# Performance work log

Measured on AMD Instinct MI355X. Metric: run time of the kernel, lower is better.

The kernel has to match this reference:

```python
import jax, jax.numpy as jnp
import numpy as np

TRIANGLE_TABLE = jnp.array([
    [-1, -1, -1, -1, -1, -1], [1, 0, 2, -1, -1, -1], [4, 0, 3, -1, -1, -1],
    [1, 4, 2, 1, 3, 4], [3, 1, 5, -1, -1, -1], [2, 3, 0, 2, 5, 3],
    [1, 4, 0, 1, 5, 4], [4, 2, 5, -1, -1, -1], [4, 5, 2, -1, -1, -1],
    [4, 1, 0, 4, 5, 1], [3, 2, 0, 3, 5, 2], [1, 3, 5, -1, -1, -1],
    [4, 1, 2, 4, 3, 1], [3, 0, 4, -1, -1, -1], [2, 0, 1, -1, -1, -1],
    [-1, -1, -1, -1, -1, -1]], dtype=jnp.int32)
NUM_TRI_TABLE = jnp.array([0, 1, 1, 2, 1, 2, 2, 1, 1, 2, 2, 1, 2, 1, 1, 0], dtype=jnp.int32)
BASE_TET_EDGES = jnp.array([0, 1, 0, 2, 0, 3, 1, 2, 1, 3, 2, 3], dtype=jnp.int32)

NUM_VERTS = 500_000
NUM_TETS = 2_000_000


def setup_inputs() -> dict:
    key = jax.random.key(0)
    k1, k2, k3 = jax.random.split(key, 3)
    pos_nx3 = jax.random.normal(k1, (NUM_VERTS, 3), dtype=jnp.float32)
    sdf_n = jax.random.normal(k2, (NUM_VERTS,), dtype=jnp.float32)
    tet_fx4 = jax.random.randint(k3, (NUM_TETS, 4), 0, NUM_VERTS)
    return {"pos_nx3": pos_nx3, "sdf_n": sdf_n, "tet_fx4": tet_fx4}


def _map_uv(face_gidx, max_idx):
    N = int(np.ceil(np.sqrt((max_idx + 1) // 2)))
    lin = jnp.linspace(0.0, 1.0 - 1.0 / N, N, dtype=jnp.float32)
    tex_y, tex_x = jnp.meshgrid(lin, lin, indexing='ij')
    pad = 0.9 / N
    # (N, N, 8) -> (N*N*4, 2): 4 uv corners per texel
    uvs = jnp.stack([tex_x, tex_y, tex_x + pad, tex_y,
                     tex_x + pad, tex_y + pad, tex_x, tex_y + pad], axis=-1).reshape(-1, 2)
    tet_idx = face_gidx // 2
    x = tet_idx % N
    y = tet_idx // N
    tet_idx = y * N + x
    tri_idx = face_gidx % 2
    uv_idx = jnp.stack([tet_idx * 4, tet_idx * 4 + tri_idx + 1,
                        tet_idx * 4 + tri_idx + 2], axis=-1).reshape(-1, 3)
    return uvs, uv_idx


def reference(pos_nx3, sdf_n, tet_fx4):
    # --- topology extraction (non-differentiable, data-dependent shapes; eager) ---
    occ_n = sdf_n > 0                                  # (N,)
    occ_fx4 = occ_n[tet_fx4]                           # (F, 4)
    occ_sum = occ_fx4.sum(-1)
    valid = (occ_sum > 0) & (occ_sum < 4)              # surface-crossing tets
    tets_v = tet_fx4[valid]                            # (Fv, 4)

    e = tets_v[:, BASE_TET_EDGES].reshape(-1, 2)       # (Fv*6, 2)
    e = jnp.stack([jnp.minimum(e[:, 0], e[:, 1]),
                   jnp.maximum(e[:, 0], e[:, 1])], axis=-1)  # sorted edges
    unique_edges, idx_map = jnp.unique(e, axis=0, return_inverse=True)
    idx_map = idx_map.reshape(-1)

    mask_edges = occ_n[unique_edges].sum(-1) == 1      # edges crossing surface
    mapping = jnp.where(mask_edges, jnp.cumsum(mask_edges) - 1, -1)
    idx_map = mapping[idx_map].reshape(-1, 6)          # (Fv, 6) per-tet edge->vert id
    interp_v = unique_edges[mask_edges]                # (E, 2)

    # --- differentiable vertex interpolation ---
    p = pos_nx3[interp_v]                              # (E, 2, 3)
    signs = jnp.array([[1.0], [-1.0]], dtype=pos_nx3.dtype)
    s = sdf_n[interp_v][..., None] * signs             # (E, 2, 1), second negated
    w = jnp.flip(s, axis=1) / s.sum(1, keepdims=True)
    verts = (p * w).sum(1)                             # (E, 3)

    # --- triangulation via lookup table ---
    v_id = jnp.array([1, 2, 4, 8], dtype=jnp.int32)
    tetindex = (occ_fx4[valid].astype(jnp.int32) * v_id).sum(-1)  # (Fv,)
    ntri = NUM_TRI_TABLE[tetindex]
    m1 = ntri == 1
    m2 = ntri == 2
    f1 = jnp.take_along_axis(idx_map[m1], TRIANGLE_TABLE[tetindex[m1]][:, :3], axis=1).reshape(-1, 3)
    f2 = jnp.take_along_axis(idx_map[m2], TRIANGLE_TABLE[tetindex[m2]][:, :6], axis=1).reshape(-1, 3)
    faces = jnp.concatenate([f1, f2], axis=0)

    num_tets = tet_fx4.shape[0]
    tet_gidx = jnp.arange(num_tets)[valid]
    g2 = tet_gidx[m2] * 2
    face_gidx = jnp.concatenate([tet_gidx[m1] * 2,
                                 jnp.stack([g2, g2 + 1], axis=-1).reshape(-1)], axis=0)
    uvs, uv_idx = _map_uv(face_gidx, num_tets * 2)
    return verts, faces, uvs, uv_idx
```

## Files before the change

### kernel.cpp

```cpp
#include <hip/hip_runtime.h>
#include <stdint.h>
#include <math.h>

#define SB 256
#define SI 8
#define SCHUNK (SB*SI)
#define C2 2048
#define LDSN (C2 + 256)
#define HEADBIT 0x40000000u
#define VMASK   0x3FFFFFFFu

__constant__ int c_tri[16][6] = {
  {-1,-1,-1,-1,-1,-1},{1,0,2,-1,-1,-1},{4,0,3,-1,-1,-1},{1,4,2,1,3,4},
  {3,1,5,-1,-1,-1},{2,3,0,2,5,3},{1,4,0,1,5,4},{4,2,5,-1,-1,-1},
  {4,5,2,-1,-1,-1},{4,1,0,4,5,1},{3,2,0,3,5,2},{1,3,5,-1,-1,-1},
  {4,1,2,4,3,1},{3,0,4,-1,-1,-1},{2,0,1,-1,-1,-1},{-1,-1,-1,-1,-1,-1}};
__constant__ int c_ntri[16] = {0,1,1,2,1,2,2,1,1,2,2,1,2,1,1,0};
__constant__ int c_ea[6] = {0,0,0,1,1,2};
__constant__ int c_eb[6] = {1,2,3,2,3,3};

__global__ void k_classify(const int4* __restrict__ tet, const float* __restrict__ sdf,
                           uint8_t* __restrict__ tetidx, int* __restrict__ bucketCnt,
                           ushort4* __restrict__ stash, int nt) {
  int t = blockIdx.x * blockDim.x + threadIdx.x;
  if (t >= nt) return;
  int4 v = tet[t];
  int ids[4] = {v.x, v.y, v.z, v.w};
  int bits = 0;
#pragma unroll
  for (int i = 0; i < 4; i++) bits |= (sdf[ids[i]] > 0.0f) ? (1 << i) : 0;
  tetidx[t] = (uint8_t)bits;
  if (c_ntri[bits] == 0) return;
  int los[4];
  int c = 0;
#pragma unroll
  for (int e = 0; e < 6; e++) {
    int a = c_ea[e], b = c_eb[e];
    if ((((bits >> a) ^ (bits >> b)) & 1) == 0) continue;
    int va = ids[a], vb = ids[b];
    los[c++] = va < vb ? va : vb;
  }
  unsigned short st[4] = {0, 0, 0, 0};
  unsigned done = 0;
#pragma unroll
  for (int i = 0; i < 4; i++) {
    if (i >= c || (done & (1u << i))) continue;
    int cnt = 1;
#pragma unroll
    for (int j = 1; j < 4; j++)
      if (i + j < c && los[i + j] == los[i]) cnt++;
    int base = atomicAdd(&bucketCnt[los[i]], cnt);
    int k = 0;
#pragma unroll
    for (int j = 0; j < 4; j++) {
      if (i + j < c && los[i + j] == los[i]) {
        st[i + j] = (unsigned short)(base + k);
        k++;
        done |= 1u << (i + j);
      }
    }
  }
  stash[t] = make_ushort4(st[0], st[1], st[2], st[3]);
}

__device__ inline unsigned long long blkExclU64(unsigned long long val, unsigned long long* sh) {
  int tid = threadIdx.x;
  sh[tid] = val; __syncthreads();
  for (int st = 1; st < SB; st <<= 1) {
    unsigned long long add = (tid >= st) ? sh[tid - st] : 0ull;
    __syncthreads();
    sh[tid] += add;
    __syncthreads();
  }
  return sh[tid] - val;
}
__device__ inline int blkExclI32(int val, int* sh) {
  int tid = threadIdx.x;
  sh[tid] = val; __syncthreads();
  for (int st = 1; st < SB; st <<= 1) {
    int add = (tid >= st) ? sh[tid - st] : 0;
    __syncthreads();
    sh[tid] += add;
    __syncthreads();
  }
  return sh[tid] - val;
}

__global__ void k_pass1(const uint8_t* __restrict__ tetidx, int nt,
                        const int* __restrict__ bucketCnt, int nv,
                        unsigned long long* __restrict__ btU, int* __restrict__ btI, int nb_t) {
  __shared__ unsigned long long shU[SB];
  int* shI = (int*)shU;
  if ((int)blockIdx.x < nb_t) {
    int base = blockIdx.x * SCHUNK + threadIdx.x * SI;
    unsigned long long s = 0;
    for (int k = 0; k < SI; k++) {
      int i = base + k;
      if (i < nt) {
        int n3 = c_ntri[tetidx[i]];
        s += (n3 == 1 ? 1ull : 0ull) + (n3 == 2 ? (1ull << 32) : 0ull);
      }
    }
    shU[threadIdx.x] = s; __syncthreads();
    for (int st = SB / 2; st > 0; st >>= 1) {
      if (threadIdx.x < st) shU[threadIdx.x] += shU[threadIdx.x + st];
      __syncthreads();
    }
    if (threadIdx.x == 0) btU[blockIdx.x] = shU[0];
  } else {
    int bid = blockIdx.x - nb_t;
    int base = bid * SCHUNK + threadIdx.x * SI;
    int s = 0;
    for (int k = 0; k < SI; k++) { int i = base + k; if (i < nv) s += bucketCnt[i]; }
    shI[threadIdx.x] = s; __syncthreads();
    for (int st = SB / 2; st > 0; st >>= 1) {
      if (threadIdx.x < st) shI[threadIdx.x] += shI[threadIdx.x + st];
      __syncthreads();
    }
    if (threadIdx.x == 0) btI[bid] = shI[0];
  }
}

__global__ void k_scanmid(unsigned long long* __restrict__ btU, int nbU,
                          int* __restrict__ btI, int nbI, int* __restrict__ scal) {
  __shared__ unsigned long long shU[SB];
  __shared__ unsigned long long carryU;
  int* shI = (int*)shU;
  __shared__ int carryI;
  if (blockIdx.x == 0) {
    if (threadIdx.x == 0) carryU = 0;
    __syncthreads();
    for (int base = 0; base < nbU; base += SB) {
      int i = base + threadIdx.x;
      unsigned long long v = (i < nbU) ? btU[i] : 0ull;
      unsigned long long ex = blkExclU64(v, shU);
      unsigned long long carry = carryU;
      if (i < nbU) btU[i] = carry + ex;
      __syncthreads();
      if (threadIdx.x == SB - 1) carryU = carry + ex + v;
      __syncthreads();
    }
    if (threadIdx.x == 0) {
      scal[0] = (int)(carryU & 0xffffffffull);
      scal[1] = (int)(carryU >> 32);
    }
  } else {
    if (threadIdx.x == 0) carryI = 0;
    __syncthreads();
    for (int base = 0; base < nbI; base += SB) {
      int i = base + threadIdx.x;
      int v = (i < nbI) ? btI[i] : 0;
      int ex = blkExclI32(v, shI);
      int carry = carryI;
      if (i < nbI) btI[i] = carry + ex;
      __syncthreads();
      if (threadIdx.x == SB - 1) carryI = carry + ex + v;
      __syncthreads();
    }
    if (threadIdx.x == 0) scal[2] = carryI;
  }
}

__global__ void k_pass3(const uint8_t* __restrict__ tetidx, int nt,
                        const int* __restrict__ bucketCnt, int nv,
                        const unsigned long long* __restrict__ btU, const int* __restrict__ btI,
                        unsigned long long* __restrict__ tetRank, int* __restrict__ bucketOff,
                        int nb_t) {
  __shared__ unsigned long long shU[SB];
  int* shI = (int*)shU;
  if ((int)blockIdx.x < nb_t) {
    int base = blockIdx.x * SCHUNK + threadIdx.x * SI;
    unsigned long long vals[SI];
    unsigned long long s = 0;
    for (int k = 0; k < SI; k++) {
      int i = base + k;
      unsigned long long v = 0;
      if (i < nt) {
        int n3 = c_ntri[tetidx[i]];
        v = (n3 == 1 ? 1ull : 0ull) + (n3 == 2 ? (1ull << 32) : 0ull);
      }
      vals[k] = s; s += v;
    }
    unsigned long long thrOff = blkExclU64(s, shU);
    unsigned long long off = btU[blockIdx.x] + thrOff;
    for (int k = 0; k < SI; k++) {
      int i = base + k;
      if (i < nt) tetRank[i] = off + vals[k];
    }
  } else {
    int bid = blockIdx.x - nb_t;
    int base = bid * SCHUNK + threadIdx.x * SI;
    int vals[SI];
    int s = 0;
    for (int k = 0; k < SI; k++) {
      int i = base + k;
      int v = (i < nv) ? bucketCnt[i] : 0;
      vals[k] = s; s += v;
    }
    int thrOff = blkExclI32(s, shI);
    int off = btI[bid] + thrOff;
    for (int k = 0; k < SI; k++) {
      int i = base + k;
      if (i < nv) bucketOff[i] = off + vals[k];
    }
  }
}

__global__ void k_i32scan1(const int* __restrict__ src, int* __restrict__ bt, int n) {
  __shared__ int sh[SB];
  int base = blockIdx.x * SCHUNK + threadIdx.x * SI;
  int s = 0;
  for (int k = 0; k < SI; k++) { int i = base + k; if (i < n) s += src[i]; }
  sh[threadIdx.x] = s; __syncthreads();
  for (int st = SB / 2; st > 0; st >>= 1) {
    if (threadIdx.x < st) sh[threadIdx.x] += sh[threadIdx.x + st];
    __syncthreads();
  }
  if (threadIdx.x == 0) bt[blockIdx.x] = sh[0];
}

__global__ void k_uscanblk(int* __restrict__ bt, int nb, int* __restrict__ scal, int uvsElems) {
  __shared__ int sh[SB];
  __shared__ int carrySh;
  if (threadIdx.x == 0) carrySh = 0;
  __syncthreads();
  for (int base = 0; base < nb; base += SB) {
    int i = base + threadIdx.x;
    int v = (i < nb) ? bt[i] : 0;
    int ex = blkExclI32(v, sh);
    int carry = carrySh;
    if (i < nb) bt[i] = carry + ex;
    __syncthreads();
    if (threadIdx.x == SB - 1) carrySh = carry + ex + v;
    __syncthreads();
  }
  if (threadIdx.x == 0) {
    int E = carrySh;
    scal[3] = E;
    int M1 = scal[0], M2 = scal[1];
    int F = M1 + 2 * M2;
    scal[4] = 3 * E;
    scal[5] = 3 * E + 3 * F;
    scal[6] = scal[5] + uvsElems;
  }
}

__global__ void k_i32scan3(const int* __restrict__ src, const int* __restrict__ bt,
                           int* __restrict__ dst, int n) {
  __shared__ int sh[SB];
  int base = blockIdx.x * SCHUNK + threadIdx.x * SI;
  int vals[SI];
  int s = 0;
  for (int k = 0; k < SI; k++) {
    int i = base + k;
    int v = (i < n) ? src[i] : 0;
    vals[k] = s; s += v;
  }
  int thrOff = blkExclI32(s, sh);
  int off = bt[blockIdx.x] + thrOff;
  for (int k = 0; k < SI; k++) {
    int i = base + k;
    if (i < n) dst[i] = off + vals[k];
  }
}

__global__ void k_scatter(const int4* __restrict__ tet, const uint8_t* __restrict__ tetidx,
                          const int* __restrict__ bucketOff, const ushort4* __restrict__ stash,
                          unsigned* __restrict__ edges32, int4* __restrict__ stashAbs, int nt) {
  int t = blockIdx.x * blockDim.x + threadIdx.x;
  if (t >= nt) return;
  int bits = tetidx[t];
  if (c_ntri[bits] == 0) return;
  int4 v = tet[t];
  int ids[4] = {v.x, v.y, v.z, v.w};
  ushort4 stv = stash[t];
  unsigned short sta[4] = {stv.x, stv.y, stv.z, stv.w};
  int sa[4] = {0, 0, 0, 0};
  int c = 0;
#pragma unroll
  for (int e = 0; e < 6; e++) {
    int a = c_ea[e], b = c_eb[e];
    if ((((bits >> a) ^ (bits >> b)) & 1) == 0) continue;
    int va = ids[a], vb = ids[b];
    int lo = va < vb ? va : vb;
    int hi = va < vb ? vb : va;
    int abs = bucketOff[lo] + (int)sta[c];
    edges32[abs] = (unsigned)hi;
    sa[c] = abs;
    c++;
  }
  stashAbs[t] = make_int4(sa[0], sa[1], sa[2], sa[3]);
}

__global__ __launch_bounds__(SB) void k_rankuniq(
    const int* __restrict__ bucketOff, const unsigned* __restrict__ edges32,
    unsigned short* __restrict__ hrankArr, unsigned* __restrict__ edgesU,
    int* __restrict__ uniqueCnt, int* __restrict__ tmpHead,
    const int* __restrict__ scal, int nv) {
  __shared__ unsigned sh[LDSN];
  __shared__ unsigned shB[LDSN];
  __shared__ int shVS, shVE;
  int totSlots = scal[2];
  long long s0 = (long long)blockIdx.x * C2;
  long long s1 = s0 + C2;
  if (threadIdx.x == 0) {
    int lo = 0, hi = nv;
    while (lo < hi) { int mid = (lo + hi) >> 1;
      long long key = (long long)bucketOff[mid] + mid;
      if (key < s0) lo = mid + 1; else hi = mid; }
    shVS = lo;
    hi = nv;
    while (lo < hi) { int mid = (lo + hi) >> 1;
      long long key = (long long)bucketOff[mid] + mid;
      if (key < s1) lo = mid + 1; else hi = mid; }
    shVE = lo;
  }
  __syncthreads();
  int vS = shVS, vE = shVE;
  if (vS >= vE) return;
  int occS = bucketOff[vS];
  int occE = (vE < nv) ? bucketOff[vE] : totSlots;
  int cnt = occE - occS;
  if (cnt <= LDSN) {
    for (int v = vS + threadIdx.x; v < vE; v += SB) {
      int o = bucketOff[v];
      int nx = (v + 1 < nv) ? bucketOff[v + 1] : totSlots;
      if (nx > o) {
        unsigned pack = ((unsigned)(o - occS) << 16) | (unsigned)(nx - occS);
        for (int k = o; k < nx; k++) shB[k - occS] = pack;
      }
    }
    for (int i = threadIdx.x; i < cnt; i += SB) sh[i] = edges32[occS + i];
    __syncthreads();
    for (int i = threadIdx.x; i < cnt; i += SB) {
      int lb = (int)(shB[i] >> 16);
      unsigned myv = sh[i] & VMASK;
      bool head = true;
      for (int k = lb; k < i; k++)
        if (((sh[k] ^ myv) & VMASK) == 0) { head = false; break; }
      if (head) sh[i] = myv | HEADBIT;
    }
    __syncthreads();
    for (int i = threadIdx.x; i < cnt; i += SB) {
      unsigned b = shB[i];
      int lb = (int)(b >> 16), le = (int)(b & 0xffffu);
      unsigned w0 = sh[i];
      unsigned myv = w0 & VMASK;
      int rank = 0;
      for (int k = lb; k < le; k++) {
        unsigned w = sh[k];
        rank += ((w & HEADBIT) != 0u && (w & VMASK) < myv) ? 1 : 0;
      }
      hrankArr[occS + i] = (unsigned short)rank;
      if (w0 & HEADBIT) edgesU[occS + lb + rank] = myv;
    }
    for (int v = vS + threadIdx.x; v < vE; v += SB) {
      int o = bucketOff[v];
      int nx = (v + 1 < nv) ? bucketOff[v + 1] : totSlots;
      int u = 0;
      for (int k = o - occS; k < nx - occS; k++) u += (sh[k] & HEADBIT) ? 1 : 0;
      uniqueCnt[v] = u;
    }
  } else {
    for (int v = vS + threadIdx.x; v < vE; v += SB) {
      int o = bucketOff[v];
      int nx = (v + 1 < nv) ? bucketOff[v + 1] : totSlots;
      int n = nx - o;
      if (n <= 0) { uniqueCnt[v] = 0; continue; }
      for (int j = 0; j < n; j++) {
        unsigned myv = edges32[o + j];
        int head = 1;
        for (int k = 0; k < j; k++) if (edges32[o + k] == myv) { head = 0; break; }
        tmpHead[o + j] = head;
      }
      int u = 0;
      for (int j = 0; j < n; j++) {
        unsigned myv = edges32[o + j];
        int rank = 0;
        for (int k = 0; k < n; k++)
          rank += (tmpHead[o + k] && edges32[o + k] < myv) ? 1 : 0;
        hrankArr[o + j] = (unsigned short)rank;
        if (tmpHead[o + j]) { edgesU[o + rank] = myv; u++; }
      }
      uniqueCnt[v] = u;
    }
  }
}

__global__ __launch_bounds__(SB) void k_verts(
    const int* __restrict__ bucketOff, const int* __restrict__ uniqueOff,
    const unsigned short* __restrict__ hrankArr, const unsigned* __restrict__ edgesU,
    unsigned* __restrict__ grank, const float* __restrict__ pos, const float* __restrict__ sdf,
    const int* __restrict__ scal, float* __restrict__ out, int nv) {
  __shared__ int shUO[SB + 1];
  __shared__ int shBO[SB + 1];
  int v0 = blockIdx.x * SB;
  int totSlots = scal[2];
  int E = scal[3];
  for (int j = threadIdx.x; j <= SB; j += SB) {
    int gv = v0 + j;
    shUO[j] = (gv < nv) ? uniqueOff[gv] : E;
    shBO[j] = (gv < nv) ? bucketOff[gv] : totSlots;
  }
  __syncthreads();
  int v = v0 + threadIdx.x;
  if (v < nv) {
    int boff = shBO[threadIdx.x];
    int bend = shBO[threadIdx.x + 1];
    int uoff = shUO[threadIdx.x];
    for (int k = boff; k < bend; k++) grank[k] = (unsigned)(uoff + (int)hrankArr[k]);
  }
  int Ustart = shUO[0];
  int Utot = shUO[SB] - Ustart;
  for (int i = threadIdx.x; i < Utot; i += SB) {
    int gi = Ustart + i;
    int lo = 0, hi = SB;
    while (hi - lo > 1) { int mid = (lo + hi) >> 1; if (shUO[mid] <= gi) lo = mid; else hi = mid; }
    int rhat = gi - shUO[lo];
    int hiV = (int)edgesU[shBO[lo] + rhat];
    int loV = v0 + lo;
    float s0 = sdf[loV];
    float ns1 = -sdf[hiV];
    float denom = s0 + ns1;
    float w0 = ns1 / denom;
    float w1 = s0 / denom;
    out[3 * gi + 0] = pos[3 * loV + 0] * w0 + pos[3 * hiV + 0] * w1;
    out[3 * gi + 1] = pos[3 * loV + 1] * w0 + pos[3 * hiV + 1] * w1;
    out[3 * gi + 2] = pos[3 * loV + 2] * w0 + pos[3 * hiV + 2] * w1;
  }
}

__global__ void k_face(const uint8_t* __restrict__ tetidx,
                       const unsigned long long* __restrict__ tetRank, const int* __restrict__ scal,
                       const int4* __restrict__ stashAbs, const unsigned* __restrict__ grank,
                       float* __restrict__ out, int nt) {
  int t = blockIdx.x * blockDim.x + threadIdx.x;
  if (t >= nt) return;
  int bits = tetidx[t];
  int nt3 = c_ntri[bits];
  if (nt3 == 0) return;
  int4 sabs = stashAbs[t];
  int sa[4] = {sabs.x, sabs.y, sabs.z, sabs.w};
  int rk[6];
  int c = 0;
#pragma unroll
  for (int e = 0; e < 6; e++) {
    int a = c_ea[e], b = c_eb[e];
    if ((((bits >> a) ^ (bits >> b)) & 1) == 0) continue;
    rk[e] = (int)grank[sa[c++]];
  }
  unsigned long long pk = tetRank[t];
  int M1 = scal[0], facesOff = scal[4], uvidxOff = scal[6];
  int row = (nt3 == 1) ? (int)(pk & 0xffffffffull) : M1 + 2 * (int)(pk >> 32);
  float* f = out + facesOff + (size_t)3 * row;
  int npos = 3 * nt3;
  for (int p = 0; p < npos; p++) f[p] = (float)rk[c_tri[bits][p]];
  float* o = out + uvidxOff + (size_t)3 * row;
  float bt4 = (float)(4 * t);
  o[0] = bt4; o[1] = bt4 + 1.0f; o[2] = bt4 + 2.0f;
  if (nt3 == 2) { o[3] = bt4; o[4] = bt4 + 2.0f; o[5] = bt4 + 3.0f; }
}

__global__ void k_uvs(const int* __restrict__ scal, float* __restrict__ out, int N) {
  int i = blockIdx.x * blockDim.x + threadIdx.x;
  int total = N * N;
  if (i >= total) return;
  int ty = i / N, tx = i - ty * N;
  float x = (float)tx / (float)N;
  float y = (float)ty / (float)N;
  float pad = (float)(0.9 / (double)N);
  float* o = out + scal[5] + (size_t)i * 8;
  o[0] = x;       o[1] = y;
  o[2] = x + pad; o[3] = y;
  o[4] = x + pad; o[5] = y + pad;
  o[6] = x;       o[7] = y + pad;
}

extern "C" void kernel_launch(void* const* d_in, const int* in_sizes, int n_in,
                              void* d_out, int out_size, void* d_ws, size_t ws_size,
                              hipStream_t stream) {
  const float* pos = (const float*)d_in[0];
  const float* sdf = (const float*)d_in[1];
  const int* tet = (const int*)d_in[2];
  int nv = in_sizes[1];
  int nt = in_sizes[2] / 4;

  char* w = (char*)d_ws;
  size_t off = 0;
  auto A = [&](size_t bytes) -> char* {
    off = (off + 255) & ~(size_t)255;
    char* p = w + off;
    off += bytes;
    return p;
  };
  int* scal = (int*)A(64 * sizeof(int));
  uint8_t* tetidx = (uint8_t*)A((size_t)nt);
  unsigned long long* tetRank = (unsigned long long*)A((size_t)nt * 8);
  int* bucketCnt = (int*)A((size_t)nv * 4);
  int* bucketOff = (int*)A((size_t)nv * 4);
  int* uniqueCnt = (int*)A((size_t)nv * 4);
  int* uniqueOff = (int*)A((size_t)nv * 4);
  ushort4* stash = (ushort4*)A((size_t)nt * 8);
  int4* stashAbs = (int4*)A((size_t)nt * 16);
  unsigned short* hrankArr = (unsigned short*)A((size_t)nt * 4 * 2);
  unsigned* grank = (unsigned*)A((size_t)nt * 4 * 4);
  unsigned* edges32 = (unsigned*)A((size_t)nt * 4 * 4);
  unsigned* edgesU = (unsigned*)A((size_t)nt * 4 * 4);
  int* tmpHead = (int*)A((size_t)nt * 4 * 4);
  unsigned long long* blockTotU = (unsigned long long*)A(8 * 4096);
  int* blockTotI = (int*)A(4 * 4096);

  hipMemsetAsync(bucketCnt, 0, (size_t)nv * 4, stream);

  int nb_t = (nt + SCHUNK - 1) / SCHUNK;
  int nb_v = (nv + SCHUNK - 1) / SCHUNK;
  int nbv_verts = (nv + SB - 1) / SB;
  long long maxKey = (long long)nt * 4 + nv;
  int nb_rank = (int)((maxKey + C2 - 1) / C2) + 1;

  k_classify<<<(nt + 255) / 256, 256, 0, stream>>>((const int4*)tet, sdf, tetidx, bucketCnt,
                                                   stash, nt);

  k_pass1<<<nb_t + nb_v, SB, 0, stream>>>(tetidx, nt, bucketCnt, nv, blockTotU, blockTotI, nb_t);
  k_scanmid<<<2, SB, 0, stream>>>(blockTotU, nb_t, blockTotI, nb_v, scal);
  k_pass3<<<nb_t + nb_v, SB, 0, stream>>>(tetidx, nt, bucketCnt, nv, blockTotU, blockTotI,
                                          tetRank, bucketOff, nb_t);

  k_scatter<<<(nt + 255) / 256, 256, 0, stream>>>((const int4*)tet, tetidx, bucketOff,
                                                  stash, edges32, stashAbs, nt);

  k_rankuniq<<<nb_rank, SB, 0, stream>>>(bucketOff, edges32, hrankArr, edgesU,
                                         uniqueCnt, tmpHead, scal, nv);

  long long maxidx = (long long)nt * 2;
  int N = (int)ceil(sqrt((double)((maxidx + 1) / 2)));
  int uvsElems = N * N * 8;

  k_i32scan1<<<nb_v, SB, 0, stream>>>(uniqueCnt, blockTotI, nv);
  k_uscanblk<<<1, SB, 0, stream>>>(blockTotI, nb_v, scal, uvsElems);
  k_i32scan3<<<nb_v, SB, 0, stream>>>(uniqueCnt, blockTotI, uniqueOff, nv);

  k_verts<<<nbv_verts, SB, 0, stream>>>(bucketOff, uniqueOff, hrankArr, edgesU, grank,
                                        pos, sdf, scal, (float*)d_out, nv);
  k_face<<<(nt + 255) / 256, 256, 0, stream>>>(tetidx, tetRank, scal,
                                               stashAbs, grank, (float*)d_out, nt);
  k_uvs<<<(N * N + 255) / 256, 256, 0, stream>>>(scal, (float*)d_out, N);
}
```

Measured before the change: 666.6 us.

## Recompute edge ranks in face kernel instead of materializing grank/stashAbs arrays

Removes the stashAbs and grank intermediate arrays. The face kernel now recomputes each edge's absolute slot from tet ids, bucketOff and stash, then derives its global rank from uniqueOff plus hrankArr. The pass-3 scan writes a 32-bit final row index instead of a 64-bit packed rank. The uvs kernel also switches to float4 stores. This trades large intermediate writes and reads for extra random gathers of bucketOff and uniqueOff in the face kernel.

Result: slower. 702.3 us (+5.4%).

```diff
diff --git a/kernel.cpp b/kernel.cpp
--- a/kernel.cpp
+++ b/kernel.cpp
@@ -164,28 +164,38 @@
 __global__ void k_pass3(const uint8_t* __restrict__ tetidx, int nt,
                         const int* __restrict__ bucketCnt, int nv,
                         const unsigned long long* __restrict__ btU, const int* __restrict__ btI,
-                        unsigned long long* __restrict__ tetRank, int* __restrict__ bucketOff,
+                        const int* __restrict__ scal,
+                        unsigned* __restrict__ rowIdx, int* __restrict__ bucketOff,
                         int nb_t) {
   __shared__ unsigned long long shU[SB];
   int* shI = (int*)shU;
   if ((int)blockIdx.x < nb_t) {
+    int M1 = scal[0];
     int base = blockIdx.x * SCHUNK + threadIdx.x * SI;
     unsigned long long vals[SI];
+    int n3s[SI];
     unsigned long long s = 0;
     for (int k = 0; k < SI; k++) {
       int i = base + k;
       unsigned long long v = 0;
+      int n3 = 0;
       if (i < nt) {
-        int n3 = c_ntri[tetidx[i]];
+        n3 = c_ntri[tetidx[i]];
         v = (n3 == 1 ? 1ull : 0ull) + (n3 == 2 ? (1ull << 32) : 0ull);
       }
+      n3s[k] = n3;
       vals[k] = s; s += v;
     }
     unsigned long long thrOff = blkExclU64(s, shU);
     unsigned long long off = btU[blockIdx.x] + thrOff;
     for (int k = 0; k < SI; k++) {
       int i = base + k;
-      if (i < nt) tetRank[i] = off + vals[k];
+      if (i < nt) {
+        unsigned long long r = off + vals[k];
+        unsigned row = (n3s[k] == 1) ? (unsigned)(r & 0xffffffffull)
+                                     : (unsigned)(M1 + 2 * (int)(r >> 32));
+        rowIdx[i] = row;
+      }
     }
   } else {
     int bid = blockIdx.x - nb_t;
@@ -266,7 +276,7 @@
 
 __global__ void k_scatter(const int4* __restrict__ tet, const uint8_t* __restrict__ tetidx,
                           const int* __restrict__ bucketOff, const ushort4* __restrict__ stash,
-                          unsigned* __restrict__ edges32, int4* __restrict__ stashAbs, int nt) {
+                          unsigned* __restrict__ edges32, int nt) {
   int t = blockIdx.x * blockDim.x + threadIdx.x;
   if (t >= nt) return;
   int bits = tetidx[t];
@@ -275,7 +285,6 @@
   int ids[4] = {v.x, v.y, v.z, v.w};
   ushort4 stv = stash[t];
   unsigned short sta[4] = {stv.x, stv.y, stv.z, stv.w};
-  int sa[4] = {0, 0, 0, 0};
   int c = 0;
 #pragma unroll
   for (int e = 0; e < 6; e++) {
@@ -284,12 +293,9 @@
     int va = ids[a], vb = ids[b];
     int lo = va < vb ? va : vb;
     int hi = va < vb ? vb : va;
-    int abs = bucketOff[lo] + (int)sta[c];
-    edges32[abs] = (unsigned)hi;
-    sa[c] = abs;
+    edges32[bucketOff[lo] + (int)sta[c]] = (unsigned)hi;
     c++;
   }
-  stashAbs[t] = make_int4(sa[0], sa[1], sa[2], sa[3]);
 }
 
 __global__ __launch_bounds__(SB) void k_rankuniq(
@@ -389,8 +395,8 @@
 
 __global__ __launch_bounds__(SB) void k_verts(
     const int* __restrict__ bucketOff, const int* __restrict__ uniqueOff,
-    const unsigned short* __restrict__ hrankArr, const unsigned* __restrict__ edgesU,
-    unsigned* __restrict__ grank, const float* __restrict__ pos, const float* __restrict__ sdf,
+    const unsigned* __restrict__ edgesU,
+    const float* __restrict__ pos, const float* __restrict__ sdf,
     const int* __restrict__ scal, float* __restrict__ out, int nv) {
   __shared__ int shUO[SB + 1];
   __shared__ int shBO[SB + 1];
@@ -403,13 +409,6 @@
     shBO[j] = (gv < nv) ? bucketOff[gv] : totSlots;
   }
   __syncthreads();
-  int v = v0 + threadIdx.x;
-  if (v < nv) {
-    int boff = shBO[threadIdx.x];
-    int bend = shBO[threadIdx.x + 1];
-    int uoff = shUO[threadIdx.x];
-    for (int k = boff; k < bend; k++) grank[k] = (unsigned)(uoff + (int)hrankArr[k]);
-  }
   int Ustart = shUO[0];
   int Utot = shUO[SB] - Ustart;
   for (int i = threadIdx.x; i < Utot; i += SB) {
@@ -430,28 +429,34 @@
   }
 }
 
-__global__ void k_face(const uint8_t* __restrict__ tetidx,
-                       const unsigned long long* __restrict__ tetRank, const int* __restrict__ scal,
-                       const int4* __restrict__ stashAbs, const unsigned* __restrict__ grank,
+__global__ void k_face(const int4* __restrict__ tet, const uint8_t* __restrict__ tetidx,
+                       const unsigned* __restrict__ rowIdx, const int* __restrict__ scal,
+                       const int* __restrict__ bucketOff, const int* __restrict__ uniqueOff,
+                       const ushort4* __restrict__ stash, const unsigned short* __restrict__ hrankArr,
                        float* __restrict__ out, int nt) {
   int t = blockIdx.x * blockDim.x + threadIdx.x;
   if (t >= nt) return;
   int bits = tetidx[t];
   int nt3 = c_ntri[bits];
   if (nt3 == 0) return;
-  int4 sabs = stashAbs[t];
-  int sa[4] = {sabs.x, sabs.y, sabs.z, sabs.w};
+  int4 v = tet[t];
+  int ids[4] = {v.x, v.y, v.z, v.w};
+  ushort4 stv = stash[t];
+  unsigned short sta[4] = {stv.x, stv.y, stv.z, stv.w};
   int rk[6];
   int c = 0;
 #pragma unroll
   for (int e = 0; e < 6; e++) {
     int a = c_ea[e], b = c_eb[e];
     if ((((bits >> a) ^ (bits >> b)) & 1) == 0) continue;
-    rk[e] = (int)grank[sa[c++]];
-  }
-  unsigned long long pk = tetRank[t];
-  int M1 = scal[0], facesOff = scal[4], uvidxOff = scal[6];
-  int row = (nt3 == 1) ? (int)(pk & 0xffffffffull) : M1 + 2 * (int)(pk >> 32);
+    int va = ids[a], vb = ids[b];
+    int lo = va < vb ? va : vb;
+    int abs = bucketOff[lo] + (int)sta[c];
+    rk[e] = uniqueOff[lo] + (int)hrankArr[abs];
+    c++;
+  }
+  int row = (int)rowIdx[t];
+  int facesOff = scal[4], uvidxOff = scal[6];
   float* f = out + facesOff + (size_t)3 * row;
   int npos = 3 * nt3;
   for (int p = 0; p < npos; p++) f[p] = (float)rk[c_tri[bits][p]];
@@ -470,10 +475,10 @@
   float y = (float)ty / (float)N;
   float pad = (float)(0.9 / (double)N);
   float* o = out + scal[5] + (size_t)i * 8;
-  o[0] = x;       o[1] = y;
-  o[2] = x + pad; o[3] = y;
-  o[4] = x + pad; o[5] = y + pad;
-  o[6] = x;       o[7] = y + pad;
+  float4 a = make_float4(x, y, x + pad, y);
+  float4 b = make_float4(x + pad, y + pad, x, y + pad);
+  *(float4*)(o) = a;
+  *(float4*)(o + 4) = b;
 }
 
 extern "C" void kernel_launch(void* const* d_in, const int* in_sizes, int n_in,
@@ -495,15 +500,13 @@
   };
   int* scal = (int*)A(64 * sizeof(int));
   uint8_t* tetidx = (uint8_t*)A((size_t)nt);
-  unsigned long long* tetRank = (unsigned long long*)A((size_t)nt * 8);
+  unsigned* rowIdx = (unsigned*)A((size_t)nt * 4);
   int* bucketCnt = (int*)A((size_t)nv * 4);
   int* bucketOff = (int*)A((size_t)nv * 4);
   int* uniqueCnt = (int*)A((size_t)nv * 4);
   int* uniqueOff = (int*)A((size_t)nv * 4);
   ushort4* stash = (ushort4*)A((size_t)nt * 8);
-  int4* stashAbs = (int4*)A((size_t)nt * 16);
   unsigned short* hrankArr = (unsigned short*)A((size_t)nt * 4 * 2);
-  unsigned* grank = (unsigned*)A((size_t)nt * 4 * 4);
   unsigned* edges32 = (unsigned*)A((size_t)nt * 4 * 4);
   unsigned* edgesU = (unsigned*)A((size_t)nt * 4 * 4);
   int* tmpHead = (int*)A((size_t)nt * 4 * 4);
@@ -524,10 +527,10 @@
   k_pass1<<<nb_t + nb_v, SB, 0, stream>>>(tetidx, nt, bucketCnt, nv, blockTotU, blockTotI, nb_t);
   k_scanmid<<<2, SB, 0, stream>>>(blockTotU, nb_t, blockTotI, nb_v, scal);
   k_pass3<<<nb_t + nb_v, SB, 0, stream>>>(tetidx, nt, bucketCnt, nv, blockTotU, blockTotI,
-                                          tetRank, bucketOff, nb_t);
+                                          scal, rowIdx, bucketOff, nb_t);
 
   k_scatter<<<(nt + 255) / 256, 256, 0, stream>>>((const int4*)tet, tetidx, bucketOff,
-                                                  stash, edges32, stashAbs, nt);
+                                                  stash, edges32, nt);
 
   k_rankuniq<<<nb_rank, SB, 0, stream>>>(bucketOff, edges32, hrankArr, edgesU,
                                          uniqueCnt, tmpHead, scal, nv);
@@ -540,9 +543,10 @@
   k_uscanblk<<<1, SB, 0, stream>>>(blockTotI, nb_v, scal, uvsElems);
   k_i32scan3<<<nb_v, SB, 0, stream>>>(uniqueCnt, blockTotI, uniqueOff, nv);
 
-  k_verts<<<nbv_verts, SB, 0, stream>>>(bucketOff, uniqueOff, hrankArr, edgesU, grank,
+  k_verts<<<nbv_verts, SB, 0, stream>>>(bucketOff, uniqueOff, edgesU,
                                         pos, sdf, scal, (float*)d_out, nv);
-  k_face<<<(nt + 255) / 256, 256, 0, stream>>>(tetidx, tetRank, scal,
-                                               stashAbs, grank, (float*)d_out, nt);
+  k_face<<<(nt + 255) / 256, 256, 0, stream>>>((const int4*)tet, tetidx, rowIdx, scal,
+                                               bucketOff, uniqueOff, stash, hrankArr,
+                                               (float*)d_out, nt);
   k_uvs<<<(N * N + 255) / 256, 256, 0, stream>>>(scal, (float*)d_out, N);
 }
```
